# Kernel optimization log

Hardware: AMD Instinct MI355X
Metric: run time of the kernel (lower is better)

The kernel has to match this reference:

```python
import jax, jax.numpy as jnp
import numpy as np

N, E, IN, H, C, L = 40000, 640000, 256, 128, 64, 4
ALPHA, LAMB = 0.5, 1.0


def setup_inputs() -> dict:
    key = jax.random.key(0)
    ks = jax.random.split(key, 8)
    x = jax.random.normal(ks[0], (N, IN), jnp.float32)
    src = jax.random.randint(ks[1], (E,), 0, N, jnp.int32)
    dst = jax.random.randint(ks[2], (E,), 0, N, jnp.int32)
    s_in = 1.0 / np.sqrt(IN)
    s_h = 1.0 / np.sqrt(H)
    fc1_w = jax.random.normal(ks[3], (IN, H), jnp.float32) * s_in
    fc1_b = jnp.zeros((H,), jnp.float32)
    W1 = jax.random.normal(ks[4], (L, H, H), jnp.float32) * s_h   # GCN2Conv weight1 per layer
    W2 = jax.random.normal(ks[5], (L, H, H), jnp.float32) * s_h   # GCN2Conv weight2 (initial-residual proj)
    bgc = jnp.zeros((L, H), jnp.float32)                          # GCN2Conv bias per layer
    fc2_w = jax.random.normal(ks[6], (H, C), jnp.float32) * s_h
    fc2_b = jnp.zeros((C,), jnp.float32)
    return dict(x=x, fc1_w=fc1_w, fc1_b=fc1_b, W1=W1, W2=W2, bgc=bgc,
                fc2_w=fc2_w, fc2_b=fc2_b, src=src, dst=dst)


def reference(x, fc1_w, fc1_b, W1, W2, bgc, fc2_w, fc2_b, src, dst):
    ones = jnp.ones((E,), x.dtype)
    # symmetric 'both' normalization: deg_out^{-1/2} on src side, deg_in^{-1/2} on dst side
    deg_out = jnp.clip(jax.ops.segment_sum(ones, src, num_segments=N), 1.0)
    deg_in = jnp.clip(jax.ops.segment_sum(ones, dst, num_segments=N), 1.0)
    norm_s = (deg_out ** -0.5)[:, None]
    norm_d = (deg_in ** -0.5)[:, None]

    # feature_preprocess: dropout (eval = identity) -> fc1 -> relu
    h0 = jax.nn.relu(x @ fc1_w + fc1_b)          # [N, H]
    h = h0
    for l in range(L):
        beta = float(np.log(LAMB / (l + 1) + 1.0))
        identity = h
        # sparse neighbor aggregation (SpMM via gather + segment_sum)
        agg = jax.ops.segment_sum((h * norm_s)[src], dst, num_segments=N) * norm_d
        feat = (1.0 - ALPHA) * agg               # smoothed features
        f0 = ALPHA * h0                          # initial residual
        rst = (1.0 - beta) * (feat + f0) + beta * (feat @ W1[l] + f0 @ W2[l]) + bgc[l]
        h = jax.nn.relu(rst + identity)          # outer residual + activation (dropout eval = identity)
    return h @ fc2_w + fc2_b                     # [N, C]
```

## Files before the change

### kernel.cpp

```cpp
#include <hip/hip_runtime.h>
#include <math.h>

#define N_NODES 40000
#define N_EDGES 640000
#define IN_F 256
#define H_F 128
#define C_F 64
#define L_LAYERS 4
#define SCAN_BLKS 157
#define N_CHUNKS 64
#define CHUNK_E 10000
#define HIST_WORDS 10000
#define XPAD 264

typedef short short8 __attribute__((ext_vector_type(8)));
typedef unsigned short ushort8 __attribute__((ext_vector_type(8)));
typedef float f32x4 __attribute__((ext_vector_type(4)));

__device__ inline short to_bf16(float f) {
    unsigned u = __builtin_bit_cast(unsigned, f);
    unsigned r = (u + 0x7FFFu + ((u >> 16) & 1u)) >> 16;
    return (short)r;
}
__device__ inline float bf16_to_f(unsigned short u) {
    unsigned v = ((unsigned)u) << 16;
    return __builtin_bit_cast(float, v);
}

__device__ inline int block_excl_scan(int v, int* wsum, int* tot) {
    int tid = threadIdx.x;
    int lane = tid & 63, wid = tid >> 6;
    int incl = v;
    #pragma unroll
    for (int off = 1; off < 64; off <<= 1) {
        int t = __shfl_up(incl, off, 64);
        if (lane >= off) incl += t;
    }
    if (lane == 63) wsum[wid] = incl;
    __syncthreads();
    int prefix = 0, total = 0;
    #pragma unroll
    for (int w = 0; w < 4; w++) {
        int s = wsum[w];
        if (w < wid) prefix += s;
        total += s;
    }
    *tot = total;
    return prefix + incl - v;
}

__global__ __launch_bounds__(256) void prep_fc1w(const float* __restrict__ fc1_w,
                                                 short* __restrict__ fc1_wT) {
    int i = blockIdx.x * 256 + threadIdx.x;
    int n = i >> 8, k = i & 255;
    fc1_wT[i] = to_bf16(fc1_w[k * H_F + n]);
}

__global__ __launch_bounds__(256) void hist_fc1_prep(const int* __restrict__ src,
                                                     const int* __restrict__ dst,
                                                     int* __restrict__ chunk_dst,
                                                     int* __restrict__ chunk_src,
                                                     unsigned char* __restrict__ lrank8,
                                                     const float* __restrict__ x,
                                                     const short* __restrict__ wT,
                                                     const float* __restrict__ b,
                                                     unsigned short* __restrict__ h0b,
                                                     const float* __restrict__ W1,
                                                     const float* __restrict__ W2,
                                                     const float* __restrict__ fc2_w,
                                                     float s0, float s1, float s2, float s3,
                                                     short* __restrict__ WcatT,
                                                     short* __restrict__ fc2_wT) {
    __shared__ union {
        int cntp[HIST_WORDS];
        unsigned short xL[64 * XPAD];
    } sh;
    int blk = blockIdx.x;
    int tid = threadIdx.x;
    if (blk < 128) {
        int role_dst = (blk < 64);
        int w = role_dst ? blk : blk - 64;
        const int* idx = role_dst ? dst : src;
        int base = w * CHUNK_E;
        for (int i = tid; i < HIST_WORDS; i += 256) sh.cntp[i] = 0;
        __syncthreads();
        if (role_dst) {
            for (int i = tid; i < CHUNK_E; i += 256) {
                int d = idx[base + i];
                int shf = (d & 3) * 8;
                int old = atomicAdd(&sh.cntp[d >> 2], 1 << shf);
                lrank8[base + i] = (unsigned char)((old >> shf) & 0xff);
            }
        } else {
            for (int i = tid; i < CHUNK_E; i += 256) {
                int s = idx[base + i];
                atomicAdd(&sh.cntp[s >> 2], 1 << ((s & 3) * 8));
            }
        }
        __syncthreads();
        int* outp = role_dst ? (chunk_dst + w * HIST_WORDS) : (chunk_src + w * HIST_WORDS);
        for (int i = tid; i < HIST_WORDS; i += 256) outp[i] = sh.cntp[i];
        return;
    }
    if (blk >= 753) {
        int i = (blk - 753) * 256 + tid;
        if (i < 4 * 128 * 256) {
            int l = i >> 15; int r = i & 32767; int n = r >> 8; int k = r & 255;
            float sc = (l == 0) ? s0 : (l == 1) ? s1 : (l == 2) ? s2 : s3;
            float w = (k < 128) ? W1[l * 16384 + k * H_F + n]
                                : W2[l * 16384 + (k - 128) * H_F + n];
            WcatT[i] = to_bf16(sc * w);
        }
        if (i < 64 * 128) {
            int n = i >> 7, k = i & 127;
            fc2_wT[i] = to_bf16(fc2_w[k * C_F + n]);
        }
        return;
    }
    int bb = blk - 128;
    const float* xblk = x + (size_t)bb * 64 * IN_F;
    #pragma unroll
    for (int half = 0; half < 2; half++) {
        float4 v[8];
        #pragma unroll
        for (int s = 0; s < 8; s++)
            v[s] = *(const float4*)(xblk + (half * 8 + s) * 1024 + tid * 4);
        #pragma unroll
        for (int s = 0; s < 8; s++) {
            int i = (half * 8 + s) * 1024 + tid * 4;
            int rr = i >> 8, cc = i & 255;
            unsigned p0 = (unsigned)(unsigned short)to_bf16(v[s].x)
                        | ((unsigned)(unsigned short)to_bf16(v[s].y) << 16);
            unsigned p1 = (unsigned)(unsigned short)to_bf16(v[s].z)
                        | ((unsigned)(unsigned short)to_bf16(v[s].w) << 16);
            uint2 pk = {p0, p1};
            *(uint2*)(sh.xL + rr * XPAD + cc) = pk;
        }
    }
    __syncthreads();
    int wave = tid >> 6, lane = tid & 63;
    int m = lane & 15, quad = lane >> 4;
    const unsigned short* xr = sh.xL + (wave * 16 + m) * XPAD + quad * 8;
    short8 afrag[8];
    #pragma unroll
    for (int ks = 0; ks < 8; ks++) {
        afrag[ks] = __builtin_bit_cast(short8, *(const ushort8*)(xr + ks * 32));
    }
    #pragma unroll
    for (int c = 0; c < 8; c += 2) {
        f32x4 acc0 = {0.f, 0.f, 0.f, 0.f};
        f32x4 acc1 = {0.f, 0.f, 0.f, 0.f};
        const short* b0p = wT + (size_t)(c * 16 + m) * IN_F + quad * 8;
        const short* b1p = b0p + 16 * IN_F;
        #pragma unroll
        for (int ks = 0; ks < 8; ks++) {
            short8 b0 = *(const short8*)(b0p + ks * 32);
            short8 b1 = *(const short8*)(b1p + ks * 32);
            acc0 = __builtin_amdgcn_mfma_f32_16x16x32_bf16(afrag[ks], b0, acc0, 0, 0, 0);
            acc1 = __builtin_amdgcn_mfma_f32_16x16x32_bf16(afrag[ks], b1, acc1, 0, 0, 0);
        }
        int col0 = c * 16 + m;
        int rbase = bb * 64 + wave * 16 + quad * 4;
        float bg0 = b[col0], bg1 = b[col0 + 16];
        #pragma unroll
        for (int r = 0; r < 4; r++) {
            size_t idx2 = (size_t)(rbase + r) * H_F + col0;
            float v0 = acc0[r] + bg0;
            float v1 = acc1[r] + bg1;
            v0 = v0 > 0.f ? v0 : 0.f;
            v1 = v1 > 0.f ? v1 : 0.f;
            h0b[idx2] = (unsigned short)to_bf16(v0);
            h0b[idx2 + 16] = (unsigned short)to_bf16(v1);
        }
    }
}

__global__ __launch_bounds__(256) void scan1(const int* __restrict__ chunk_dst,
                                             const int* __restrict__ chunk_src,
                                             int* __restrict__ base32,
                                             float* __restrict__ rsq_in,
                                             float* __restrict__ rsq_out,
                                             float* __restrict__ sq_out,
                                             int* __restrict__ row_local,
                                             int* __restrict__ blk_sum) {
    __shared__ int wsum[4];
    int sb = blockIdx.x;
    int n = sb * 256 + threadIdx.x;
    int deg = 0, word = 0, sh = 0;
    if (n < N_NODES) {
        word = n >> 2; sh = (n & 3) * 8;
        #pragma unroll 4
        for (int w = 0; w < N_CHUNKS; w++)
            deg += (chunk_dst[w * HIST_WORDS + word] >> sh) & 0xff;
    }
    int tot;
    int excl = block_excl_scan(deg, wsum, &tot);
    if (n < N_NODES) {
        row_local[n] = excl;
        int run = excl;
        #pragma unroll 4
        for (int w = 0; w < N_CHUNKS; w++) {
            int v = (chunk_dst[w * HIST_WORDS + word] >> sh) & 0xff;
            base32[(size_t)w * N_NODES + n] = run;
            run += v;
        }
        int so = 0;
        #pragma unroll 4
        for (int w = 0; w < N_CHUNKS; w++)
            so += (chunk_src[w * HIST_WORDS + word] >> sh) & 0xff;
        float fd = (float)(deg < 1 ? 1 : deg);
        float fs = (float)(so < 1 ? 1 : so);
        rsq_in[n] = 1.0f / sqrtf(fd);
        rsq_out[n] = 1.0f / sqrtf(fs);
        sq_out[n] = sqrtf(fs);
    }
    if (threadIdx.x == 0) blk_sum[sb] = tot;
}

__global__ __launch_bounds__(256) void fill_fused(const int* __restrict__ src,
                                                  const int* __restrict__ dst,
                                                  const unsigned char* __restrict__ lrank8,
                                                  const int* __restrict__ base32,
                                                  const int* __restrict__ row_local,
                                                  const int* __restrict__ blk_sum,
                                                  unsigned short* __restrict__ col16,
                                                  int* __restrict__ row_ptr,
                                                  const unsigned short* __restrict__ h0b,
                                                  const float* __restrict__ rsq_out,
                                                  unsigned short* __restrict__ h0s) {
    __shared__ int wsum[4];
    __shared__ int blk_offL[SCAN_BLKS];
    int tid = threadIdx.x;
    {
        int v = (tid < SCAN_BLKS) ? blk_sum[tid] : 0;
        int tot;
        int excl = block_excl_scan(v, wsum, &tot);
        if (tid < SCAN_BLKS) blk_offL[tid] = excl;
    }
    __syncthreads();

    int blk = blockIdx.x;
    if (blk < 2500) {
        int e = blk * 256 + tid;
        int w = e / CHUNK_E;
        int s = src[e], d = dst[e];
        int rp = blk_offL[d >> 8] + base32[(size_t)w * N_NODES + d] + (int)lrank8[e];
        col16[rp] = (unsigned short)s;
        return;
    }
    if (blk < 2657) {
        int n = (blk - 2500) * 256 + tid;
        if (n < N_NODES) row_ptr[n] = blk_offL[n >> 8] + row_local[n];
        if (blk == 2500 && tid == 0) row_ptr[N_NODES] = N_EDGES;
        return;
    }
    int j = (blk - 2657) * 2048 + tid * 8;
    ushort8 u = *(const ushort8*)(h0b + j);
    float rs = rsq_out[j >> 7];
    ushort8 o;
    #pragma unroll
    for (int jj = 0; jj < 8; jj++) o[jj] = (unsigned short)to_bf16(rs * bf16_to_f(u[jj]));
    *(ushort8*)(h0s + j) = o;
}

__global__ __launch_bounds__(256) void spmm_kernel(const unsigned short* __restrict__ hs,
                                                   const int* __restrict__ row_ptr,
                                                   const unsigned short* __restrict__ col16,
                                                   const float* __restrict__ rsq_in,
                                                   unsigned short* __restrict__ aggb) {
    int wave = threadIdx.x >> 6, lane = threadIdx.x & 63;
    int slot = lane >> 4, fi = lane & 15;
    int n = blockIdx.x * 4 + wave;
    int e0 = row_ptr[n], e1 = row_ptr[n + 1];
    float a[8] = {};
    for (int e = e0 + slot; e < e1; e += 16) {
        int eb = e + 4, ec = e + 8, ed = e + 12;
        int c0 = col16[e];
        int c1 = (eb < e1) ? col16[eb] : c0;  float w1 = (eb < e1) ? 1.f : 0.f;
        int c2 = (ec < e1) ? col16[ec] : c0;  float w2 = (ec < e1) ? 1.f : 0.f;
        int c3 = (ed < e1) ? col16[ed] : c0;  float w3 = (ed < e1) ? 1.f : 0.f;
        ushort8 u0 = *(const ushort8*)(hs + (size_t)c0 * H_F + fi * 8);
        ushort8 u1 = *(const ushort8*)(hs + (size_t)c1 * H_F + fi * 8);
        ushort8 u2 = *(const ushort8*)(hs + (size_t)c2 * H_F + fi * 8);
        ushort8 u3 = *(const ushort8*)(hs + (size_t)c3 * H_F + fi * 8);
        #pragma unroll
        for (int j = 0; j < 8; j++) {
            a[j] += bf16_to_f(u0[j]) + w1 * bf16_to_f(u1[j])
                  + w2 * bf16_to_f(u2[j]) + w3 * bf16_to_f(u3[j]);
        }
    }
    #pragma unroll
    for (int mask = 16; mask <= 32; mask <<= 1) {
        #pragma unroll
        for (int j = 0; j < 8; j++) a[j] += __shfl_xor(a[j], mask, 64);
    }
    if (slot == 0) {
        float rs = rsq_in[n];
        ushort8 r;
        #pragma unroll
        for (int j = 0; j < 8; j++) r[j] = (unsigned short)to_bf16(rs * a[j]);
        *(ushort8*)(aggb + (size_t)n * H_F + fi * 8) = r;
    }
}

__global__ __launch_bounds__(256) void combine_mfma(const unsigned short* __restrict__ aggb,
                                                    const unsigned short* __restrict__ h0b,
                                                    const unsigned short* __restrict__ hs_in,
                                                    const short* __restrict__ wT,
                                                    const float* __restrict__ bgc,
                                                    const float* __restrict__ rsq_out,
                                                    const float* __restrict__ sq_out,
                                                    float omb5,
                                                    unsigned short* __restrict__ hs_out) {
    int tid = threadIdx.x;
    int wave = tid >> 6, lane = tid & 63;
    int rowgrp = wave >> 1, chalf = wave & 1;
    int m = lane & 15, quad = lane >> 4;
    int row = blockIdx.x * 32 + rowgrp * 16 + m;
    const unsigned short* aggr = aggb + (size_t)row * H_F + quad * 8;
    const unsigned short* h0r  = h0b + (size_t)row * H_F + quad * 8;
    short8 afrag[8];
    #pragma unroll
    for (int ks = 0; ks < 4; ks++) {
        afrag[ks] = __builtin_bit_cast(short8, *(const ushort8*)(aggr + ks * 32));
        afrag[ks + 4] = __builtin_bit_cast(short8, *(const ushort8*)(h0r + ks * 32));
    }
    #pragma unroll
    for (int ci = 0; ci < 4; ci += 2) {
        int c = chalf * 4 + ci;
        f32x4 acc0 = {0.f, 0.f, 0.f, 0.f};
        f32x4 acc1 = {0.f, 0.f, 0.f, 0.f};
        const short* b0p = wT + (size_t)(c * 16 + m) * 256 + quad * 8;
        const short* b1p = b0p + 16 * 256;
        #pragma unroll
        for (int ks = 0; ks < 8; ks++) {
            short8 b0 = *(const short8*)(b0p + ks * 32);
            short8 b1 = *(const short8*)(b1p + ks * 32);
            acc0 = __builtin_amdgcn_mfma_f32_16x16x32_bf16(afrag[ks], b0, acc0, 0, 0, 0);
            acc1 = __builtin_amdgcn_mfma_f32_16x16x32_bf16(afrag[ks], b1, acc1, 0, 0, 0);
        }
        int col0 = c * 16 + m;
        int rbase = blockIdx.x * 32 + rowgrp * 16 + quad * 4;
        float bg0 = bgc[col0], bg1 = bgc[col0 + 16];
        #pragma unroll
        for (int r = 0; r < 4; r++) {
            int rw = rbase + r;
            size_t idx = (size_t)rw * H_F + col0;
            float sq = sq_out[rw];
            float rsq = rsq_out[rw];
            float s0 = bf16_to_f(aggb[idx]) + bf16_to_f(h0b[idx]);
            float s1 = bf16_to_f(aggb[idx + 16]) + bf16_to_f(h0b[idx + 16]);
            float v0 = omb5 * s0 + acc0[r] + bg0 + sq * bf16_to_f(hs_in[idx]);
            float v1 = omb5 * s1 + acc1[r] + bg1 + sq * bf16_to_f(hs_in[idx + 16]);
            v0 = v0 > 0.f ? v0 : 0.f;
            v1 = v1 > 0.f ? v1 : 0.f;
            hs_out[idx] = (unsigned short)to_bf16(rsq * v0);
            hs_out[idx + 16] = (unsigned short)to_bf16(rsq * v1);
        }
    }
}

__global__ __launch_bounds__(256) void fc2_mfma(const unsigned short* __restrict__ hs,
                                                const float* __restrict__ sq_out,
                                                const short* __restrict__ wT,
                                                const float* __restrict__ b,
                                                float* __restrict__ out) {
    int tid = threadIdx.x;
    int wave = tid >> 6, lane = tid & 63;
    int m = lane & 15, quad = lane >> 4;
    int row = blockIdx.x * 64 + wave * 16 + m;
    const unsigned short* hr = hs + (size_t)row * H_F + quad * 8;
    float sq = sq_out[row];
    short8 afrag[4];
    #pragma unroll
    for (int ks = 0; ks < 4; ks++) {
        ushort8 u = *(const ushort8*)(hr + ks * 32);
        #pragma unroll
        for (int j = 0; j < 8; j++) afrag[ks][j] = to_bf16(sq * bf16_to_f(u[j]));
    }
    #pragma unroll
    for (int c = 0; c < 4; c += 2) {
        f32x4 acc0 = {0.f, 0.f, 0.f, 0.f};
        f32x4 acc1 = {0.f, 0.f, 0.f, 0.f};
        const short* b0p = wT + (size_t)(c * 16 + m) * H_F + quad * 8;
        const short* b1p = b0p + 16 * H_F;
        #pragma unroll
        for (int ks = 0; ks < 4; ks++) {
            short8 b0 = *(const short8*)(b0p + ks * 32);
            short8 b1 = *(const short8*)(b1p + ks * 32);
            acc0 = __builtin_amdgcn_mfma_f32_16x16x32_bf16(afrag[ks], b0, acc0, 0, 0, 0);
            acc1 = __builtin_amdgcn_mfma_f32_16x16x32_bf16(afrag[ks], b1, acc1, 0, 0, 0);
        }
        int col0 = c * 16 + m;
        int rbase = blockIdx.x * 64 + wave * 16 + quad * 4;
        float bg0 = b[col0], bg1 = b[col0 + 16];
        #pragma unroll
        for (int r = 0; r < 4; r++) {
            size_t idx = (size_t)(rbase + r) * C_F + col0;
            out[idx] = acc0[r] + bg0;
            out[idx + 16] = acc1[r] + bg1;
        }
    }
}

extern "C" void kernel_launch(void* const* d_in, const int* in_sizes, int n_in,
                              void* d_out, int out_size, void* d_ws, size_t ws_size,
                              hipStream_t stream) {
    const float* x     = (const float*)d_in[0];
    const float* fc1_w = (const float*)d_in[1];
    const float* fc1_b = (const float*)d_in[2];
    const float* W1    = (const float*)d_in[3];
    const float* W2    = (const float*)d_in[4];
    const float* bgc   = (const float*)d_in[5];
    const float* fc2_w = (const float*)d_in[6];
    const float* fc2_b = (const float*)d_in[7];
    const int*   src   = (const int*)d_in[8];
    const int*   dst   = (const int*)d_in[9];
    float* out = (float*)d_out;

    char* p = (char*)d_ws;
    auto alloc = [&](size_t bytes) {
        char* r = p;
        p += (bytes + 255) & ~(size_t)255;
        return r;
    };
    int*   chunk_dst = (int*)alloc((size_t)N_CHUNKS * HIST_WORDS * 4);
    int*   chunk_src = (int*)alloc((size_t)N_CHUNKS * HIST_WORDS * 4);
    int*   base32    = (int*)alloc((size_t)N_CHUNKS * N_NODES * 4);
    unsigned char* lrank8 = (unsigned char*)alloc((size_t)N_EDGES);
    float* rsq_in  = (float*)alloc((size_t)N_NODES * 4);
    float* rsq_out = (float*)alloc((size_t)N_NODES * 4);
    float* sq_out  = (float*)alloc((size_t)N_NODES * 4);
    int*   row_ptr   = (int*)alloc((size_t)(N_NODES + 1) * 4);
    int*   row_local = (int*)alloc((size_t)N_NODES * 4);
    int*   blk_sum   = (int*)alloc((size_t)SCAN_BLKS * 4);
    unsigned short* col16 = (unsigned short*)alloc((size_t)N_EDGES * 2);
    unsigned short* aggb = (unsigned short*)alloc((size_t)N_NODES * H_F * 2);
    unsigned short* h0b  = (unsigned short*)alloc((size_t)N_NODES * H_F * 2);
    unsigned short* h0s  = (unsigned short*)alloc((size_t)N_NODES * H_F * 2);
    unsigned short* hAs  = (unsigned short*)alloc((size_t)N_NODES * H_F * 2);
    unsigned short* hBs  = (unsigned short*)alloc((size_t)N_NODES * H_F * 2);
    short* fc1_wT  = (short*)alloc((size_t)128 * 256 * 2);
    short* WcatT   = (short*)alloc((size_t)4 * 128 * 256 * 2);
    short* fc2_wT  = (short*)alloc((size_t)64 * 128 * 2);

    float beta[4], wscale[4], omb5[4];
    for (int l = 0; l < 4; l++) {
        beta[l] = (float)log(1.0 / (double)(l + 1) + 1.0);
        wscale[l] = 0.5f * beta[l];
        omb5[l] = 0.5f * (1.f - beta[l]);
    }

    prep_fc1w<<<128, 256, 0, stream>>>(fc1_w, fc1_wT);
    hist_fc1_prep<<<1265, 256, 0, stream>>>(src, dst, chunk_dst, chunk_src, lrank8,
                                            x, fc1_wT, fc1_b, h0b,
                                            W1, W2, fc2_w,
                                            wscale[0], wscale[1], wscale[2], wscale[3],
                                            WcatT, fc2_wT);
    scan1<<<SCAN_BLKS, 256, 0, stream>>>(chunk_dst, chunk_src, base32,
                                         rsq_in, rsq_out, sq_out, row_local, blk_sum);
    fill_fused<<<5157, 256, 0, stream>>>(src, dst, lrank8, base32, row_local, blk_sum,
                                         col16, row_ptr, h0b, rsq_out, h0s);

    const unsigned short* sp_in[4] = {h0s, hAs, hBs, hAs};
    unsigned short* out_b[4]       = {hAs, hBs, hAs, hBs};
    for (int l = 0; l < L_LAYERS; l++) {
        spmm_kernel<<<N_NODES / 4, 256, 0, stream>>>(sp_in[l], row_ptr, col16,
                                                     rsq_in, aggb);
        combine_mfma<<<N_NODES / 32, 256, 0, stream>>>(aggb, h0b, sp_in[l],
                                                       WcatT + (size_t)l * 128 * 256,
                                                       bgc + (size_t)l * H_F,
                                                       rsq_out, sq_out, omb5[l],
                                                       out_b[l]);
    }
    fc2_mfma<<<N_NODES / 64, 256, 0, stream>>>(hBs, sq_out, fc2_wT, fc2_b, out);
}
```

Measured before the change: 364.4 us.

## Fuse SpMM aggregation with MFMA combine per layer and fold fc2 into last layer

Each layer's SpMM gather and dense MFMA combine now run in a single kernel. The aggregated rows for 16 nodes stay in LDS instead of round-tripping through a global bf16 buffer. On the last layer the pre-scaled activations are also written to LDS and fc2 is applied in place, removing the separate fc2 kernel and its read of the final hidden state. This cuts launches and global traffic, but each block now covers only 16 rows, so every block reloads the full weight matrix, and the irregular SpMM phase and the MFMA phase are serialised behind a barrier.

```diff
diff --git a/kernel.cpp b/kernel.cpp
--- a/kernel.cpp
+++ b/kernel.cpp
@@ -12,6 +12,7 @@
 #define CHUNK_E 10000
 #define HIST_WORDS 10000
 #define XPAD 264
+#define LPAD 132
 
 typedef short short8 __attribute__((ext_vector_type(8)));
 typedef unsigned short ushort8 __attribute__((ext_vector_type(8)));
@@ -263,71 +264,75 @@
     *(ushort8*)(h0s + j) = o;
 }
 
-__global__ __launch_bounds__(256) void spmm_kernel(const unsigned short* __restrict__ hs,
+__global__ __launch_bounds__(256) void layer_fused(const unsigned short* __restrict__ hs_in,
+                                                   const unsigned short* __restrict__ h0b,
                                                    const int* __restrict__ row_ptr,
                                                    const unsigned short* __restrict__ col16,
                                                    const float* __restrict__ rsq_in,
-                                                   unsigned short* __restrict__ aggb) {
-    int wave = threadIdx.x >> 6, lane = threadIdx.x & 63;
-    int slot = lane >> 4, fi = lane & 15;
-    int n = blockIdx.x * 4 + wave;
-    int e0 = row_ptr[n], e1 = row_ptr[n + 1];
-    float a[8] = {};
-    for (int e = e0 + slot; e < e1; e += 16) {
-        int eb = e + 4, ec = e + 8, ed = e + 12;
-        int c0 = col16[e];
-        int c1 = (eb < e1) ? col16[eb] : c0;  float w1 = (eb < e1) ? 1.f : 0.f;
-        int c2 = (ec < e1) ? col16[ec] : c0;  float w2 = (ec < e1) ? 1.f : 0.f;
-        int c3 = (ed < e1) ? col16[ed] : c0;  float w3 = (ed < e1) ? 1.f : 0.f;
-        ushort8 u0 = *(const ushort8*)(hs + (size_t)c0 * H_F + fi * 8);
-        ushort8 u1 = *(const ushort8*)(hs + (size_t)c1 * H_F + fi * 8);
-        ushort8 u2 = *(const ushort8*)(hs + (size_t)c2 * H_F + fi * 8);
-        ushort8 u3 = *(const ushort8*)(hs + (size_t)c3 * H_F + fi * 8);
-        #pragma unroll
-        for (int j = 0; j < 8; j++) {
-            a[j] += bf16_to_f(u0[j]) + w1 * bf16_to_f(u1[j])
-                  + w2 * bf16_to_f(u2[j]) + w3 * bf16_to_f(u3[j]);
-        }
-    }
-    #pragma unroll
-    for (int mask = 16; mask <= 32; mask <<= 1) {
-        #pragma unroll
-        for (int j = 0; j < 8; j++) a[j] += __shfl_xor(a[j], mask, 64);
-    }
-    if (slot == 0) {
-        float rs = rsq_in[n];
-        ushort8 r;
-        #pragma unroll
-        for (int j = 0; j < 8; j++) r[j] = (unsigned short)to_bf16(rs * a[j]);
-        *(ushort8*)(aggb + (size_t)n * H_F + fi * 8) = r;
-    }
-}
-
-__global__ __launch_bounds__(256) void combine_mfma(const unsigned short* __restrict__ aggb,
-                                                    const unsigned short* __restrict__ h0b,
-                                                    const unsigned short* __restrict__ hs_in,
-                                                    const short* __restrict__ wT,
-                                                    const float* __restrict__ bgc,
-                                                    const float* __restrict__ rsq_out,
-                                                    const float* __restrict__ sq_out,
-                                                    float omb5,
-                                                    unsigned short* __restrict__ hs_out) {
+                                                   const float* __restrict__ rsq_out,
+                                                   const float* __restrict__ sq_out,
+                                                   const short* __restrict__ wT,
+                                                   const float* __restrict__ bgc,
+                                                   float omb5,
+                                                   unsigned short* __restrict__ hs_out,
+                                                   const short* __restrict__ fc2_wT,
+                                                   const float* __restrict__ fc2_b,
+                                                   float* __restrict__ out) {
+    __shared__ unsigned short aggL[16 * LPAD];
+    __shared__ unsigned short vL[16 * LPAD];
     int tid = threadIdx.x;
     int wave = tid >> 6, lane = tid & 63;
-    int rowgrp = wave >> 1, chalf = wave & 1;
+    int slot = lane >> 4, fi = lane & 15;
+    int nodebase = blockIdx.x * 16;
+
+    #pragma unroll
+    for (int i = 0; i < 4; i++) {
+        int rl = wave * 4 + i;
+        int n = nodebase + rl;
+        int e0 = row_ptr[n], e1 = row_ptr[n + 1];
+        float a[8] = {};
+        for (int e = e0 + slot; e < e1; e += 16) {
+            int eb = e + 4, ec = e + 8, ed = e + 12;
+            int c0 = col16[e];
+            int c1 = (eb < e1) ? col16[eb] : c0;  float w1 = (eb < e1) ? 1.f : 0.f;
+            int c2 = (ec < e1) ? col16[ec] : c0;  float w2 = (ec < e1) ? 1.f : 0.f;
+            int c3 = (ed < e1) ? col16[ed] : c0;  float w3 = (ed < e1) ? 1.f : 0.f;
+            ushort8 u0 = *(const ushort8*)(hs_in + (size_t)c0 * H_F + fi * 8);
+            ushort8 u1 = *(const ushort8*)(hs_in + (size_t)c1 * H_F + fi * 8);
+            ushort8 u2 = *(const ushort8*)(hs_in + (size_t)c2 * H_F + fi * 8);
+            ushort8 u3 = *(const ushort8*)(hs_in + (size_t)c3 * H_F + fi * 8);
+            #pragma unroll
+            for (int j = 0; j < 8; j++) {
+                a[j] += bf16_to_f(u0[j]) + w1 * bf16_to_f(u1[j])
+                      + w2 * bf16_to_f(u2[j]) + w3 * bf16_to_f(u3[j]);
+            }
+        }
+        #pragma unroll
+        for (int mask = 16; mask <= 32; mask <<= 1) {
+            #pragma unroll
+            for (int j = 0; j < 8; j++) a[j] += __shfl_xor(a[j], mask, 64);
+        }
+        if (slot == 0) {
+            float rs = rsq_in[n];
+            ushort8 r;
+            #pragma unroll
+            for (int j = 0; j < 8; j++) r[j] = (unsigned short)to_bf16(rs * a[j]);
+            *(ushort8*)(aggL + rl * LPAD + fi * 8) = r;
+        }
+    }
+    __syncthreads();
+
     int m = lane & 15, quad = lane >> 4;
-    int row = blockIdx.x * 32 + rowgrp * 16 + m;
-    const unsigned short* aggr = aggb + (size_t)row * H_F + quad * 8;
-    const unsigned short* h0r  = h0b + (size_t)row * H_F + quad * 8;
-    short8 afrag[8];
-    #pragma unroll
-    for (int ks = 0; ks < 4; ks++) {
-        afrag[ks] = __builtin_bit_cast(short8, *(const ushort8*)(aggr + ks * 32));
-        afrag[ks + 4] = __builtin_bit_cast(short8, *(const ushort8*)(h0r + ks * 32));
-    }
-    #pragma unroll
-    for (int ci = 0; ci < 4; ci += 2) {
-        int c = chalf * 4 + ci;
+    {
+        const unsigned short* aggr = aggL + m * LPAD + quad * 8;
+        const unsigned short* h0r  = h0b + (size_t)(nodebase + m) * H_F + quad * 8;
+        short8 afrag[8];
+        #pragma unroll
+        for (int ks = 0; ks < 4; ks++) {
+            afrag[ks] = __builtin_bit_cast(short8, *(const ushort8*)(aggr + ks * 32));
+            afrag[ks + 4] = __builtin_bit_cast(short8, *(const ushort8*)(h0r + ks * 32));
+        }
+        int c = wave * 2;
         f32x4 acc0 = {0.f, 0.f, 0.f, 0.f};
         f32x4 acc1 = {0.f, 0.f, 0.f, 0.f};
         const short* b0p = wT + (size_t)(c * 16 + m) * 256 + quad * 8;
@@ -340,65 +345,51 @@
             acc1 = __builtin_amdgcn_mfma_f32_16x16x32_bf16(afrag[ks], b1, acc1, 0, 0, 0);
         }
         int col0 = c * 16 + m;
-        int rbase = blockIdx.x * 32 + rowgrp * 16 + quad * 4;
         float bg0 = bgc[col0], bg1 = bgc[col0 + 16];
         #pragma unroll
         for (int r = 0; r < 4; r++) {
-            int rw = rbase + r;
+            int rl = quad * 4 + r;
+            int rw = nodebase + rl;
             size_t idx = (size_t)rw * H_F + col0;
             float sq = sq_out[rw];
             float rsq = rsq_out[rw];
-            float s0 = bf16_to_f(aggb[idx]) + bf16_to_f(h0b[idx]);
-            float s1 = bf16_to_f(aggb[idx + 16]) + bf16_to_f(h0b[idx + 16]);
+            float s0 = bf16_to_f(aggL[rl * LPAD + col0]) + bf16_to_f(h0b[idx]);
+            float s1 = bf16_to_f(aggL[rl * LPAD + col0 + 16]) + bf16_to_f(h0b[idx + 16]);
             float v0 = omb5 * s0 + acc0[r] + bg0 + sq * bf16_to_f(hs_in[idx]);
             float v1 = omb5 * s1 + acc1[r] + bg1 + sq * bf16_to_f(hs_in[idx + 16]);
             v0 = v0 > 0.f ? v0 : 0.f;
             v1 = v1 > 0.f ? v1 : 0.f;
             hs_out[idx] = (unsigned short)to_bf16(rsq * v0);
             hs_out[idx + 16] = (unsigned short)to_bf16(rsq * v1);
-        }
-    }
-}
-
-__global__ __launch_bounds__(256) void fc2_mfma(const unsigned short* __restrict__ hs,
-                                                const float* __restrict__ sq_out,
-                                                const short* __restrict__ wT,
-                                                const float* __restrict__ b,
-                                                float* __restrict__ out) {
-    int tid = threadIdx.x;
-    int wave = tid >> 6, lane = tid & 63;
-    int m = lane & 15, quad = lane >> 4;
-    int row = blockIdx.x * 64 + wave * 16 + m;
-    const unsigned short* hr = hs + (size_t)row * H_F + quad * 8;
-    float sq = sq_out[row];
-    short8 afrag[4];
-    #pragma unroll
-    for (int ks = 0; ks < 4; ks++) {
-        ushort8 u = *(const ushort8*)(hr + ks * 32);
-        #pragma unroll
-        for (int j = 0; j < 8; j++) afrag[ks][j] = to_bf16(sq * bf16_to_f(u[j]));
-    }
-    #pragma unroll
-    for (int c = 0; c < 4; c += 2) {
-        f32x4 acc0 = {0.f, 0.f, 0.f, 0.f};
-        f32x4 acc1 = {0.f, 0.f, 0.f, 0.f};
-        const short* b0p = wT + (size_t)(c * 16 + m) * H_F + quad * 8;
-        const short* b1p = b0p + 16 * H_F;
+            if (out) {
+                vL[rl * LPAD + col0] = (unsigned short)to_bf16(v0);
+                vL[rl * LPAD + col0 + 16] = (unsigned short)to_bf16(v1);
+            }
+        }
+    }
+
+    if (out) {
+        __syncthreads();
+        const unsigned short* vr = vL + m * LPAD + quad * 8;
+        short8 afrag[4];
         #pragma unroll
         for (int ks = 0; ks < 4; ks++) {
-            short8 b0 = *(const short8*)(b0p + ks * 32);
-            short8 b1 = *(const short8*)(b1p + ks * 32);
-            acc0 = __builtin_amdgcn_mfma_f32_16x16x32_bf16(afrag[ks], b0, acc0, 0, 0, 0);
-            acc1 = __builtin_amdgcn_mfma_f32_16x16x32_bf16(afrag[ks], b1, acc1, 0, 0, 0);
+            afrag[ks] = __builtin_bit_cast(short8, *(const ushort8*)(vr + ks * 32));
+        }
+        int c = wave;
+        f32x4 acc = {0.f, 0.f, 0.f, 0.f};
+        const short* bp = fc2_wT + (size_t)(c * 16 + m) * H_F + quad * 8;
+        #pragma unroll
+        for (int ks = 0; ks < 4; ks++) {
+            short8 b0 = *(const short8*)(bp + ks * 32);
+            acc = __builtin_amdgcn_mfma_f32_16x16x32_bf16(afrag[ks], b0, acc, 0, 0, 0);
         }
         int col0 = c * 16 + m;
-        int rbase = blockIdx.x * 64 + wave * 16 + quad * 4;
-        float bg0 = b[col0], bg1 = b[col0 + 16];
+        float bg = fc2_b[col0];
         #pragma unroll
         for (int r = 0; r < 4; r++) {
-            size_t idx = (size_t)(rbase + r) * C_F + col0;
-            out[idx] = acc0[r] + bg0;
-            out[idx + 16] = acc1[r] + bg1;
+            int rw = nodebase + quad * 4 + r;
+            out[(size_t)rw * C_F + col0] = acc[r] + bg;
         }
     }
 }
@@ -435,7 +426,6 @@
     int*   row_local = (int*)alloc((size_t)N_NODES * 4);
     int*   blk_sum   = (int*)alloc((size_t)SCAN_BLKS * 4);
     unsigned short* col16 = (unsigned short*)alloc((size_t)N_EDGES * 2);
-    unsigned short* aggb = (unsigned short*)alloc((size_t)N_NODES * H_F * 2);
     unsigned short* h0b  = (unsigned short*)alloc((size_t)N_NODES * H_F * 2);
     unsigned short* h0s  = (unsigned short*)alloc((size_t)N_NODES * H_F * 2);
     unsigned short* hAs  = (unsigned short*)alloc((size_t)N_NODES * H_F * 2);
@@ -465,13 +455,14 @@
     const unsigned short* sp_in[4] = {h0s, hAs, hBs, hAs};
     unsigned short* out_b[4]       = {hAs, hBs, hAs, hBs};
     for (int l = 0; l < L_LAYERS; l++) {
-        spmm_kernel<<<N_NODES / 4, 256, 0, stream>>>(sp_in[l], row_ptr, col16,
-                                                     rsq_in, aggb);
-        combine_mfma<<<N_NODES / 32, 256, 0, stream>>>(aggb, h0b, sp_in[l],
-                                                       WcatT + (size_t)l * 128 * 256,
-                                                       bgc + (size_t)l * H_F,
-                                                       rsq_out, sq_out, omb5[l],
-                                                       out_b[l]);
-    }
-    fc2_mfma<<<N_NODES / 64, 256, 0, stream>>>(hBs, sq_out, fc2_wT, fc2_b, out);
-}
+        int last = (l == L_LAYERS - 1);
+        layer_fused<<<N_NODES / 16, 256, 0, stream>>>(sp_in[l], h0b, row_ptr, col16,
+                                                      rsq_in, rsq_out, sq_out,
+                                                      WcatT + (size_t)l * 128 * 256,
+                                                      bgc + (size_t)l * H_F,
+                                                      omb5[l], out_b[l],
+                                                      last ? fc2_wT : (const short*)nullptr,
+                                                      last ? fc2_b : (const float*)nullptr,
+                                                      last ? out : (float*)nullptr);
+    }
+}
```

New measurement: 359.0 us, median of 2. No clear change (-1.5%).
